# Kernel tuning notes

Measured on AMD Instinct MI355X. Metric: run time of the kernel, lower is better.

The kernel has to match this reference:

```python
import jax, jax.numpy as jnp
import numpy as np

B, N, C_S, C_COND, C_Z, H = 2, 512, 1024, 512, 128, 16
D = C_S // H  # head dim = 64
INF = 1.0e8
EPS = 1e-5


def _ln(x, scale=None, bias=None):
    m = x.mean(-1, keepdims=True)
    v = ((x - m) ** 2).mean(-1, keepdims=True)
    y = (x - m) * jax.lax.rsqrt(v + EPS)
    if scale is not None:
        y = y * scale + bias
    return y


def setup_inputs() -> dict:
    key = jax.random.key(0)
    ks = jax.random.split(key, 16)
    s = 0.02
    return {
        'x': jax.random.normal(ks[0], (B, N, C_S), jnp.float32),
        'cond': jax.random.normal(ks[1], (B, N, C_COND), jnp.float32),
        'z': jax.random.normal(ks[2], (B, N, N, C_Z), jnp.float32),
        'x_mask': jnp.ones((B, N), jnp.float32),
        # AdaLN(c_s, c_cond): scale/shift from cond
        'gamma_w': jax.random.normal(ks[3], (C_COND, C_S), jnp.float32) * s,
        'gamma_b': jnp.zeros((C_S,), jnp.float32),
        'beta_w': jax.random.normal(ks[4], (C_COND, C_S), jnp.float32) * s,
        # ln_z affine
        'z_scale': jnp.ones((C_Z,), jnp.float32),
        'z_bias': jnp.zeros((C_Z,), jnp.float32),
        # projections (all bias-free per module)
        'w_q': jax.random.normal(ks[5], (C_S, H * D), jnp.float32) * s,
        'w_kv': jax.random.normal(ks[6], (C_S, 2 * H * D), jnp.float32) * s,
        'w_b': jax.random.normal(ks[7], (C_Z, H), jnp.float32) * s,
        'w_og': jax.random.normal(ks[8], (C_S, C_S), jnp.float32) * s,
        'w_out': jax.random.normal(ks[9], (C_S, C_S), jnp.float32) * s,
        # cond_gate has bias, init -2.0
        'w_cg': jax.random.normal(ks[10], (C_COND, C_S), jnp.float32) * s,
        'b_cg': jnp.full((C_S,), -2.0, jnp.float32),
        # Transition (SwiGLU, n=2)
        'ffn_scale': jnp.ones((C_S,), jnp.float32),
        'ffn_bias': jnp.zeros((C_S,), jnp.float32),
        'w_a': jax.random.normal(ks[11], (C_S, 2 * C_S), jnp.float32) * s,
        'w_b2': jax.random.normal(ks[12], (C_S, 2 * C_S), jnp.float32) * s,
        'w_o': jax.random.normal(ks[13], (2 * C_S, C_S), jnp.float32) * s,
    }


def reference(x, cond, z, x_mask, gamma_w, gamma_b, beta_w, z_scale, z_bias,
              w_q, w_kv, w_b, w_og, w_out, w_cg, b_cg,
              ffn_scale, ffn_bias, w_a, w_b2, w_o):
    # AdaLN: LN(x, no affine) modulated by cond (sigmoid-gated scale + shift)
    cond_n = _ln(cond)
    _x = _ln(x) * jax.nn.sigmoid(cond_n @ gamma_w + gamma_b) + cond_n @ beta_w
    _z = _ln(z, z_scale, z_bias)

    q = (_x @ w_q).reshape(B, N, H, D)
    kv = _x @ w_kv
    k = kv[..., :H * D].reshape(B, N, H, D)
    v = kv[..., H * D:].reshape(B, N, H, D)

    # pair bias [B,N,N,H] -> [B,H,Nq,Nk], plus additive mask (query & key)
    b = _z @ w_b
    b = b + INF * (x_mask[:, None, :, None] - 1.0)  # key mask
    b = b + INF * (x_mask[:, :, None, None] - 1.0)  # query mask
    bias = jnp.transpose(b, (0, 3, 1, 2))  # [B,H,Nq,Nk]

    scale = 1.0 / jnp.sqrt(jnp.asarray(D, x.dtype))
    scores = jnp.einsum('bqhd,bkhd->bhqk', q, k) * scale + bias
    attn = jax.nn.softmax(scores, axis=-1)
    update = jnp.einsum('bhqk,bkhd->bqhd', attn, v).reshape(B, N, C_S)

    update = (update * jax.nn.sigmoid(_x @ w_og)) @ w_out
    update = update * jax.nn.sigmoid(cond @ w_cg + b_cg)
    x = x + update  # dropout is identity in eval

    # Transition (SwiGLU, n=2), masked residual
    xl = _ln(x, ffn_scale, ffn_bias)
    ffn = (jax.nn.silu(xl @ w_a) * (xl @ w_b2)) @ w_o
    x = x + ffn * x_mask[..., None]
    return x
```

## Files before the change

kernel.cpp:

```cpp
#include <hip/hip_runtime.h>
#include <stdint.h>

typedef unsigned short u16;
typedef unsigned int u32;
typedef __attribute__((ext_vector_type(4))) float f32x4;
typedef __attribute__((ext_vector_type(4))) unsigned int u32x4;
typedef __attribute__((ext_vector_type(4))) unsigned short u16x4;
typedef __attribute__((ext_vector_type(8))) __bf16 bf16x8;

union Frag { u32x4 u; bf16x8 b; };

__device__ __forceinline__ u16 f2bf(float x) {
  u32 u = __float_as_uint(x);
  u32 r = (u + 0x7fffu + ((u >> 16) & 1u)) >> 16;
  return (u16)r;
}
__device__ __forceinline__ float bf2f(u16 v) {
  u32 u = ((u32)v) << 16;
  return __uint_as_float(u);
}
__device__ __forceinline__ float sigmoidf_(float x) { return 1.0f / (1.0f + __expf(-x)); }

__device__ __forceinline__ void gload16(const void* g, void* lds) {
  __builtin_amdgcn_global_load_lds((const __attribute__((address_space(1))) unsigned int*)g,
                                   (__attribute__((address_space(3))) unsigned int*)lds, 16, 0, 0);
}

template<int EPI, int MI>
__device__ __forceinline__ void gemm_body(int bx, int by,
                                          u16* As0, u16* As1, u16* Bs0, u16* Bs1,
                                          const u16* __restrict__ A, const u16* __restrict__ Bt,
                                          const float* __restrict__ bias,
                                          const float* __restrict__ e0, const float* __restrict__ e1,
                                          void* __restrict__ Cp, int M, int N, int K) {
  constexpr int BM = 32 * MI;
  const int t = threadIdx.x, wave = t >> 6, lane = t & 63;
  const int lrow = lane & 15, lgrp = lane >> 4;
  const int m0 = bx * BM, n0 = by * 128;
  const int wr = (wave >> 1) * (16 * MI), wc = (wave & 1) * 64;

  const int srow = wave * 8 + (lane >> 3);
  const int scol = (((lane & 7) ^ (lane >> 3)) << 3);
  const u16* Ab = A + (size_t)(m0 + srow) * K + scol;
  const u16* Bb = Bt + (size_t)(n0 + srow) * K + scol;

  f32x4 acc[MI][4] = {};

  auto stage = [&](int k0, u16* Asd, u16* Bsd) {
#pragma unroll
    for (int i = 0; i < MI; ++i) gload16(Ab + (size_t)i * 32 * K + k0, Asd + wave * 512 + i * 2048);
#pragma unroll
    for (int i = 0; i < 4; ++i) gload16(Bb + (size_t)i * 32 * K + k0, Bsd + wave * 512 + i * 2048);
  };
  auto compute = [&](const u16* Asr, const u16* Bsr) {
#pragma unroll
    for (int ks = 0; ks < 2; ++ks) {
      Frag af[MI], bf4[4];
#pragma unroll
      for (int mi = 0; mi < MI; ++mi) {
        int row = wr + mi * 16 + lrow;
        int slot = ((ks << 2) + lgrp) ^ (row & 7);
        af[mi].u = *(const u32x4*)((const char*)Asr + row * 128 + (slot << 4));
      }
#pragma unroll
      for (int ni = 0; ni < 4; ++ni) {
        int row = wc + ni * 16 + lrow;
        int slot = ((ks << 2) + lgrp) ^ (row & 7);
        bf4[ni].u = *(const u32x4*)((const char*)Bsr + row * 128 + (slot << 4));
      }
#pragma unroll
      for (int mi = 0; mi < MI; ++mi)
#pragma unroll
        for (int ni = 0; ni < 4; ++ni)
          acc[mi][ni] = __builtin_amdgcn_mfma_f32_16x16x32_bf16(af[mi].b, bf4[ni].b, acc[mi][ni], 0, 0, 0);
    }
  };

  stage(0, As0, Bs0);
  __syncthreads();
  for (int k0 = 0; k0 < K; k0 += 128) {
    stage(k0 + 64, As1, Bs1);
    compute(As0, Bs0);
    __syncthreads();
    if (k0 + 128 < K) stage(k0 + 128, As0, Bs0);
    compute(As1, Bs1);
    __syncthreads();
  }

  if constexpr (EPI == 4 || EPI == 5) {
    const int half = N >> 1;
#pragma unroll
    for (int mi = 0; mi < MI; ++mi) {
#pragma unroll
      for (int np = 0; np < 2; ++np) {
        int j = ((n0 + wc) >> 1) + np * 16 + lrow;
        float bj = 0.0f;
        if (EPI == 5) bj = bias[j];
#pragma unroll
        for (int rg = 0; rg < 4; ++rg) {
          int row = m0 + wr + mi * 16 + lgrp * 4 + rg;
          float a = acc[mi][2 * np][rg];
          float b = acc[mi][2 * np + 1][rg];
          float val;
          if constexpr (EPI == 4) {
            val = a * sigmoidf_(a) * b;
          } else {
            float mean = e1[2 * row], rinv = e1[2 * row + 1];
            float lnx = (e0[(size_t)row * half + j] - mean) * rinv;
            val = lnx * sigmoidf_(a + bj) + b;
          }
          ((u16*)Cp)[(size_t)row * half + j] = f2bf(val);
        }
      }
    }
  } else if constexpr (EPI == 6) {
    u16* vTp = (u16*)bias;
    const bool isv = (n0 >= 2048) && (n0 < 3072);
#pragma unroll
    for (int mi = 0; mi < MI; ++mi) {
#pragma unroll
      for (int ni = 0; ni < 4; ++ni) {
        int col = n0 + wc + ni * 16 + lrow;
        int rowb = m0 + wr + mi * 16 + lgrp * 4;
        if (isv) {
          int h = (col - 2048) >> 6, d = col & 63;
          int b = rowb >> 9, n = rowb & 511;
          u16x4 o;
#pragma unroll
          for (int rg = 0; rg < 4; ++rg) o[rg] = f2bf(acc[mi][ni][rg]);
          *(u16x4*)(vTp + ((size_t)((b * 16 + h) * 64 + d)) * 512 + n) = o;
        } else {
#pragma unroll
          for (int rg = 0; rg < 4; ++rg)
            ((u16*)Cp)[(size_t)(rowb + rg) * N + col] = f2bf(acc[mi][ni][rg]);
        }
      }
    }
  } else {
#pragma unroll
    for (int mi = 0; mi < MI; ++mi) {
#pragma unroll
      for (int ni = 0; ni < 4; ++ni) {
        int col = n0 + wc + ni * 16 + lrow;
        float bv = 0.0f;
        if (EPI == 0 && bias) bv = bias[col];
#pragma unroll
        for (int rg = 0; rg < 4; ++rg) {
          int row = m0 + wr + mi * 16 + lgrp * 4 + rg;
          size_t idx = (size_t)row * N + col;
          float v = acc[mi][ni][rg];
          if constexpr (EPI == 0)      ((float*)Cp)[idx] = v + bv;
          else if constexpr (EPI == 1) ((u16*)Cp)[idx] = f2bf(v);
          else if constexpr (EPI == 2) ((float*)Cp)[idx] = e0[idx] + v * sigmoidf_(e1[idx]);
          else                         ((float*)Cp)[idx] = e0[idx] + v * e1[row];
        }
      }
    }
  }
  (void)M;
}

template<int EPI, int MI>
__global__ __launch_bounds__(256) void gemm_t(const u16* __restrict__ A, const u16* __restrict__ Bt,
                                              const float* __restrict__ bias,
                                              const float* __restrict__ e0, const float* __restrict__ e1,
                                              void* __restrict__ Cp, int M, int N, int K) {
  __shared__ u16 As0[32 * MI * 64], As1[32 * MI * 64];
  __shared__ u16 Bs0[128 * 64], Bs1[128 * 64];
  gemm_body<EPI, MI>(blockIdx.x, blockIdx.y, As0, As1, Bs0, Bs1, A, Bt, bias, e0, e1, Cp, M, N, K);
}

__global__ __launch_bounds__(256) void gemm_adaln_cg(
    const u16* __restrict__ cnb, const u16* __restrict__ gbT, const float* __restrict__ gamma_b,
    const float* __restrict__ x, const float* __restrict__ xstat, u16* __restrict__ xbf,
    const u16* __restrict__ cb, const u16* __restrict__ cgT, const float* __restrict__ b_cg,
    float* __restrict__ cglin) {
  __shared__ u16 As0[64 * 64], As1[64 * 64];
  __shared__ u16 Bs0[128 * 64], Bs1[128 * 64];
  int id = blockIdx.x;
  if (id < 256) {
    gemm_body<5, 2>(id & 15, id >> 4, As0, As1, Bs0, Bs1, cnb, gbT, gamma_b, x, xstat, xbf, 1024, 2048, 512);
  } else {
    id -= 256;
    gemm_body<0, 1>(id & 31, id >> 5, As0, As1, Bs0, Bs1, cb, cgT, b_cg, nullptr, nullptr, cglin, 1024, 1024, 512);
  }
}

__device__ __forceinline__ void wtrans_body(
    int id, float (*T)[65],
    const float* __restrict__ gamma_w, const float* __restrict__ beta_w,
    const float* __restrict__ w_cg, const float* __restrict__ w_q,
    const float* __restrict__ w_kv, const float* __restrict__ w_og,
    const float* __restrict__ w_out, const float* __restrict__ w_a,
    const float* __restrict__ w_b2, const float* __restrict__ w_o,
    u16* __restrict__ gbT, u16* __restrict__ cgT, u16* __restrict__ qkvT,
    u16* __restrict__ woT, u16* __restrict__ abT, u16* __restrict__ oT) {
  const float* src; u16* dst; int K, N, ptype = 0;
  if (id < 128)       { src = gamma_w; dst = gbT;  K = 512;  N = 1024; ptype = 1; }
  else if (id < 256)  { src = beta_w;  dst = gbT;  K = 512;  N = 1024; ptype = 2; id -= 128; }
  else if (id < 384)  { src = w_cg;    dst = cgT;  K = 512;  N = 1024; id -= 256; }
  else if (id < 640)  { src = w_q;     dst = qkvT; K = 1024; N = 1024; id -= 384; }
  else if (id < 1152) { src = w_kv;    dst = qkvT + (size_t)1024 * 1024; K = 1024; N = 2048; id -= 640; }
  else if (id < 1408) { src = w_og;    dst = qkvT + (size_t)3072 * 1024; K = 1024; N = 1024; id -= 1152; }
  else if (id < 1664) { src = w_out;   dst = woT;  K = 1024; N = 1024; id -= 1408; }
  else if (id < 2176) { src = w_a;     dst = abT;  K = 1024; N = 2048; ptype = 1; id -= 1664; }
  else if (id < 2688) { src = w_b2;    dst = abT;  K = 1024; N = 2048; ptype = 2; id -= 2176; }
  else                { src = w_o;     dst = oT;   K = 2048; N = 1024; id -= 2688; }
  const int tk = K >> 6;
  const int k0 = (id % tk) * 64, n0 = (id / tk) * 64;

  const int t = threadIdx.x;
#pragma unroll
  for (int i = 0; i < 4; ++i) {
    int idx = i * 256 + t;
    int kr = idx >> 4, c4 = (idx & 15) << 2;
    f32x4 v = *(const f32x4*)(src + (size_t)(k0 + kr) * N + n0 + c4);
    T[kr][c4] = v.x; T[kr][c4 + 1] = v.y; T[kr][c4 + 2] = v.z; T[kr][c4 + 3] = v.w;
  }
  __syncthreads();
#pragma unroll
  for (int i = 0; i < 2; ++i) {
    int idx = i * 256 + t;
    int n = idx >> 3, kc = (idx & 7) << 3;
    u32x4 o;
#pragma unroll
    for (int j = 0; j < 4; ++j) {
      u16 lo = f2bf(T[kc + 2 * j][n]);
      u16 hi = f2bf(T[kc + 2 * j + 1][n]);
      o[j] = (u32)lo | ((u32)hi << 16);
    }
    int ng = n0 + n;
    int r = (ptype == 0) ? ng : (((ng >> 4) << 5) + (ng & 15) + ((ptype == 2) ? 16 : 0));
    *(u32x4*)(dst + (size_t)r * K + k0 + kc) = o;
  }
}

__device__ __forceinline__ void block_reduce2_256(float& s, float& q, float* sb, int t) {
#pragma unroll
  for (int m = 1; m < 64; m <<= 1) { s += __shfl_xor(s, m); q += __shfl_xor(q, m); }
  if ((t & 63) == 0) { sb[(t >> 6) * 2] = s; sb[(t >> 6) * 2 + 1] = q; }
  __syncthreads();
  s = sb[0] + sb[2] + sb[4] + sb[6];
  q = sb[1] + sb[3] + sb[5] + sb[7];
}

__device__ __forceinline__ void ln_cond_x_body(int row, const float* __restrict__ cond,
                                               const float* __restrict__ x,
                                               u16* __restrict__ cnb, u16* __restrict__ cb,
                                               float* __restrict__ xstat) {
  const int t = threadIdx.x;
  __shared__ float sb[8];
  f32x4 xv = *(const f32x4*)(x + (size_t)row * 1024 + t * 4);
  float s = xv.x + xv.y + xv.z + xv.w;
  float q = xv.x * xv.x + xv.y * xv.y + xv.z * xv.z + xv.w * xv.w;
  block_reduce2_256(s, q, sb, t);
  if (t == 0) {
    float mean = s * (1.0f / 1024.0f);
    float var = q * (1.0f / 1024.0f) - mean * mean;
    xstat[2 * row] = mean;
    xstat[2 * row + 1] = rsqrtf(var + 1e-5f);
  }
  __syncthreads();
  f32x4 cv = {0.0f, 0.0f, 0.0f, 0.0f};
  if (t < 128) cv = *(const f32x4*)(cond + (size_t)row * 512 + t * 4);
  float s2 = cv.x + cv.y + cv.z + cv.w;
  float q2 = cv.x * cv.x + cv.y * cv.y + cv.z * cv.z + cv.w * cv.w;
  block_reduce2_256(s2, q2, sb, t);
  if (t < 128) {
    float mean = s2 * (1.0f / 512.0f);
    float var = q2 * (1.0f / 512.0f) - mean * mean;
    float rinv = rsqrtf(var + 1e-5f);
    u16x4 on, oc;
    on.x = f2bf((cv.x - mean) * rinv); on.y = f2bf((cv.y - mean) * rinv);
    on.z = f2bf((cv.z - mean) * rinv); on.w = f2bf((cv.w - mean) * rinv);
    oc.x = f2bf(cv.x); oc.y = f2bf(cv.y); oc.z = f2bf(cv.z); oc.w = f2bf(cv.w);
    *(u16x4*)(cnb + (size_t)row * 512 + t * 4) = on;
    *(u16x4*)(cb + (size_t)row * 512 + t * 4) = oc;
  }
}

__device__ __forceinline__ void biasz_body(int bq, const float* __restrict__ z,
                                           const float* __restrict__ zs, const float* __restrict__ zbias,
                                           const float* __restrict__ wb, const float* __restrict__ xmask,
                                           u16* __restrict__ biasb) {
  const int b = bq >> 9, qi = bq & 511;
  const int t = threadIdx.x, wave = t >> 6, lane = t & 63;
  const int lrow = lane & 15, lgrp = lane >> 4;

  float zsv[32], zbv[32];
  Frag wf[4];
#pragma unroll
  for (int j = 0; j < 4; ++j) {
#pragma unroll
    for (int e2 = 0; e2 < 4; ++e2) {
      int c0 = 32 * j + lgrp * 8 + e2 * 2;
      zsv[j * 8 + e2 * 2] = zs[c0];
      zsv[j * 8 + e2 * 2 + 1] = zs[c0 + 1];
      zbv[j * 8 + e2 * 2] = zbias[c0];
      zbv[j * 8 + e2 * 2 + 1] = zbias[c0 + 1];
      u16 lo = f2bf(wb[c0 * 16 + lrow]);
      u16 hi = f2bf(wb[(c0 + 1) * 16 + lrow]);
      wf[j].u[e2] = (u32)lo | ((u32)hi << 16);
    }
  }
  float qm = xmask[b * 512 + qi];
  float qadd = 1.0e8f * (qm - 1.0f);
  const float* zrowbase = z + ((size_t)(b * 512 + qi)) * 512 * 128;

  for (int kt = wave; kt < 32; kt += 4) {
    const float* zp = zrowbase + (size_t)(kt * 16 + lrow) * 128;
    float zv[32];
#pragma unroll
    for (int j = 0; j < 4; ++j) {
      f32x4 v0 = *(const f32x4*)(zp + 32 * j + lgrp * 8);
      f32x4 v1 = *(const f32x4*)(zp + 32 * j + lgrp * 8 + 4);
      zv[j * 8 + 0] = v0.x; zv[j * 8 + 1] = v0.y; zv[j * 8 + 2] = v0.z; zv[j * 8 + 3] = v0.w;
      zv[j * 8 + 4] = v1.x; zv[j * 8 + 5] = v1.y; zv[j * 8 + 6] = v1.z; zv[j * 8 + 7] = v1.w;
    }
    float s = 0.0f, q2 = 0.0f;
#pragma unroll
    for (int i = 0; i < 32; ++i) { s += zv[i]; q2 += zv[i] * zv[i]; }
    s += __shfl_xor(s, 16); q2 += __shfl_xor(q2, 16);
    s += __shfl_xor(s, 32); q2 += __shfl_xor(q2, 32);
    float mean = s * (1.0f / 128.0f);
    float var = q2 * (1.0f / 128.0f) - mean * mean;
    float rinv = rsqrtf(var + 1e-5f);

    f32x4 acc = {0.0f, 0.0f, 0.0f, 0.0f};
#pragma unroll
    for (int j = 0; j < 4; ++j) {
      Frag afr;
#pragma unroll
      for (int e2 = 0; e2 < 4; ++e2) {
        float zn0 = (zv[j * 8 + e2 * 2] - mean) * rinv * zsv[j * 8 + e2 * 2] + zbv[j * 8 + e2 * 2];
        float zn1 = (zv[j * 8 + e2 * 2 + 1] - mean) * rinv * zsv[j * 8 + e2 * 2 + 1] + zbv[j * 8 + e2 * 2 + 1];
        afr.u[e2] = (u32)f2bf(zn0) | ((u32)f2bf(zn1) << 16);
      }
      acc = __builtin_amdgcn_mfma_f32_16x16x32_bf16(afr.b, wf[j].b, acc, 0, 0, 0);
    }

    int kbase = kt * 16 + lgrp * 4;
    float v0 = acc[0] + qadd + 1.0e8f * (xmask[b * 512 + kbase + 0] - 1.0f);
    float v1 = acc[1] + qadd + 1.0e8f * (xmask[b * 512 + kbase + 1] - 1.0f);
    float v2 = acc[2] + qadd + 1.0e8f * (xmask[b * 512 + kbase + 2] - 1.0f);
    float v3 = acc[3] + qadd + 1.0e8f * (xmask[b * 512 + kbase + 3] - 1.0f);
    u16* outp = biasb + (((size_t)(b * 16 + lrow) * 512 + qi) * 512 + kbase);
    *(u32*)outp       = (u32)f2bf(v0) | ((u32)f2bf(v1) << 16);
    *(u32*)(outp + 2) = (u32)f2bf(v2) | ((u32)f2bf(v3) << 16);
  }
}

__global__ __launch_bounds__(256) void mega0(
    const float* __restrict__ z, const float* __restrict__ zs, const float* __restrict__ zbias,
    const float* __restrict__ wb, const float* __restrict__ xmask, u16* __restrict__ biasb,
    const float* __restrict__ gamma_w, const float* __restrict__ beta_w,
    const float* __restrict__ w_cg, const float* __restrict__ w_q,
    const float* __restrict__ w_kv, const float* __restrict__ w_og,
    const float* __restrict__ w_out, const float* __restrict__ w_a,
    const float* __restrict__ w_b2, const float* __restrict__ w_o,
    u16* __restrict__ gbT, u16* __restrict__ cgT, u16* __restrict__ qkvT,
    u16* __restrict__ woT, u16* __restrict__ abT, u16* __restrict__ oT,
    const float* __restrict__ cond, const float* __restrict__ x,
    u16* __restrict__ cnb, u16* __restrict__ cb, float* __restrict__ xstat) {
  __shared__ float Tsh[64][65];
  int id = blockIdx.x;
  if (id < 1024) {
    biasz_body(id, z, zs, zbias, wb, xmask, biasb);
  } else if (id < 4224) {
    wtrans_body(id - 1024, Tsh, gamma_w, beta_w, w_cg, w_q, w_kv, w_og, w_out, w_a, w_b2, w_o,
                gbT, cgT, qkvT, woT, abT, oT);
  } else {
    ln_cond_x_body(id - 4224, cond, x, cnb, cb, xstat);
  }
}

__global__ __launch_bounds__(256) void attn(const u16* __restrict__ qkv, const u16* __restrict__ vT,
                                            const u16* __restrict__ biasb, u16* __restrict__ gub) {
  __shared__ u16 Ks[64 * 64];
  __shared__ u16 Vs[64 * 64];
  __shared__ u16 Ps[4][16 * 64];
  __shared__ u16 Bbs[64 * 64];
  const int t = threadIdx.x, wave = t >> 6, lane = t & 63;
  const int lrow = lane & 15, lgrp = lane >> 4;
  const int bh = blockIdx.x >> 3, qt = blockIdx.x & 7;
  const int b = bh >> 4, h = bh & 15;
  const int q0 = qt * 64 + wave * 16;

  Frag qf[2];
#pragma unroll
  for (int ks = 0; ks < 2; ++ks) {
    int tok = b * 512 + q0 + lrow;
    qf[ks].u = *(const u32x4*)(qkv + (size_t)tok * 4096 + h * 64 + ks * 32 + lgrp * 8);
  }
  f32x4 oacc[4] = {};
  float mrun[4], lrun[4];
#pragma unroll
  for (int rg = 0; rg < 4; ++rg) { mrun[rg] = -3.0e38f; lrun[rg] = 0.0f; }

  const int o0 = t * 16, o1 = 4096 + t * 16;
  const int r0 = o0 >> 7, s0 = (o0 >> 4) & 7;
  const int r1 = o1 >> 7, s1 = (o1 >> 4) & 7;
  const int c0 = (s0 ^ (r0 & 7)) << 3;
  const int c1 = (s1 ^ (r1 & 7)) << 3;
  const int br0 = t >> 3, bs0 = t & 7;
  const int br1 = 32 + (t >> 3);
  const u16* bbase = biasb + ((size_t)bh * 512 + qt * 64) * 512;

  const u16* kp0 = qkv + (size_t)(b * 512 + r0) * 4096 + 1024 + h * 64 + c0;
  const u16* kp1 = qkv + (size_t)(b * 512 + r1) * 4096 + 1024 + h * 64 + c1;
  const u16* vp0 = vT + (size_t)(bh * 64 + r0) * 512 + c0;
  const u16* vp1 = vT + (size_t)(bh * 64 + r1) * 512 + c1;
  const u16* bp0 = bbase + (size_t)br0 * 512 + bs0 * 8;
  const u16* bp1 = bbase + (size_t)br1 * 512 + bs0 * 8;

  u32x4 kv0 = *(const u32x4*)(kp0);
  u32x4 kv1 = *(const u32x4*)(kp1);
  u32x4 vv0 = *(const u32x4*)(vp0);
  u32x4 vv1 = *(const u32x4*)(vp1);
  u32x4 bb0 = *(const u32x4*)(bp0);
  u32x4 bb1 = *(const u32x4*)(bp1);

  for (int kt = 0; kt < 8; ++kt) {
    __syncthreads();
    *(u32x4*)((char*)Ks + o0) = kv0;
    *(u32x4*)((char*)Ks + o1) = kv1;
    *(u32x4*)((char*)Vs + o0) = vv0;
    *(u32x4*)((char*)Vs + o1) = vv1;
    *(u32x4*)((char*)Bbs + br0 * 128 + ((bs0 ^ (br0 & 7)) << 4)) = bb0;
    *(u32x4*)((char*)Bbs + br1 * 128 + ((bs0 ^ (br1 & 7)) << 4)) = bb1;
    __syncthreads();

    {
      int k1g = ((kt + 1) & 7) * 64;
      kv0 = *(const u32x4*)(kp0 + (size_t)k1g * 4096);
      kv1 = *(const u32x4*)(kp1 + (size_t)k1g * 4096);
      vv0 = *(const u32x4*)(vp0 + k1g);
      vv1 = *(const u32x4*)(vp1 + k1g);
      bb0 = *(const u32x4*)(bp0 + k1g);
      bb1 = *(const u32x4*)(bp1 + k1g);
    }

    f32x4 sf[4] = {};
#pragma unroll
    for (int ks = 0; ks < 2; ++ks) {
#pragma unroll
      for (int ni = 0; ni < 4; ++ni) {
        int row = ni * 16 + lrow;
        int slot = (ks * 4 + lgrp) ^ (row & 7);
        Frag kf;
        kf.u = *(const u32x4*)((const char*)Ks + row * 128 + (slot << 4));
        sf[ni] = __builtin_amdgcn_mfma_f32_16x16x32_bf16(qf[ks].b, kf.b, sf[ni], 0, 0, 0);
      }
    }

    float sv[4][4];
#pragma unroll
    for (int ni = 0; ni < 4; ++ni) {
#pragma unroll
      for (int rg = 0; rg < 4; ++rg) {
        int qlocal = wave * 16 + lgrp * 4 + rg;
        int k = ni * 16 + lrow;
        float bvv = bf2f(*(const u16*)((const char*)Bbs + qlocal * 128 +
                                       (((k >> 3) ^ (qlocal & 7)) << 4) + (k & 7) * 2));
        sv[ni][rg] = sf[ni][rg] * 0.125f + bvv;
      }
    }
    float mnew[4], fac[4];
#pragma unroll
    for (int rg = 0; rg < 4; ++rg) {
      float tm = fmaxf(fmaxf(sv[0][rg], sv[1][rg]), fmaxf(sv[2][rg], sv[3][rg]));
      tm = fmaxf(tm, __shfl_xor(tm, 1));
      tm = fmaxf(tm, __shfl_xor(tm, 2));
      tm = fmaxf(tm, __shfl_xor(tm, 4));
      tm = fmaxf(tm, __shfl_xor(tm, 8));
      mnew[rg] = fmaxf(mrun[rg], tm);
      fac[rg] = __expf(mrun[rg] - mnew[rg]);
      mrun[rg] = mnew[rg];
    }
    float psum[4] = {0.0f, 0.0f, 0.0f, 0.0f};
#pragma unroll
    for (int ni = 0; ni < 4; ++ni)
#pragma unroll
      for (int rg = 0; rg < 4; ++rg) {
        float p = __expf(sv[ni][rg] - mnew[rg]);
        sv[ni][rg] = p;
        psum[rg] += p;
      }
#pragma unroll
    for (int rg = 0; rg < 4; ++rg) {
      float ps = psum[rg];
      ps += __shfl_xor(ps, 1); ps += __shfl_xor(ps, 2);
      ps += __shfl_xor(ps, 4); ps += __shfl_xor(ps, 8);
      lrun[rg] = lrun[rg] * fac[rg] + ps;
#pragma unroll
      for (int nd = 0; nd < 4; ++nd) oacc[nd][rg] *= fac[rg];
    }
#pragma unroll
    for (int ni = 0; ni < 4; ++ni)
#pragma unroll
      for (int rg = 0; rg < 4; ++rg) {
        int prow = lgrp * 4 + rg;
        int col = ni * 16 + lrow;
        int slot = (col >> 3) ^ (prow & 7);
        *(u16*)((char*)Ps[wave] + prow * 128 + (slot << 4) + (col & 7) * 2) = f2bf(sv[ni][rg]);
      }
    Frag paf[2];
#pragma unroll
    for (int ks = 0; ks < 2; ++ks) {
      int slot = (ks * 4 + lgrp) ^ (lrow & 7);
      paf[ks].u = *(const u32x4*)((const char*)Ps[wave] + lrow * 128 + (slot << 4));
    }
#pragma unroll
    for (int ks = 0; ks < 2; ++ks)
#pragma unroll
      for (int nd = 0; nd < 4; ++nd) {
        int row = nd * 16 + lrow;
        int slot = (ks * 4 + lgrp) ^ (row & 7);
        Frag vf;
        vf.u = *(const u32x4*)((const char*)Vs + row * 128 + (slot << 4));
        oacc[nd] = __builtin_amdgcn_mfma_f32_16x16x32_bf16(paf[ks].b, vf.b, oacc[nd], 0, 0, 0);
      }
  }

#pragma unroll
  for (int nd = 0; nd < 4; ++nd) {
#pragma unroll
    for (int rg = 0; rg < 4; ++rg) {
      int tok = b * 512 + q0 + lgrp * 4 + rg;
      int col = h * 64 + nd * 16 + lrow;
      float og = bf2f(qkv[(size_t)tok * 4096 + 3072 + col]);
      float val = oacc[nd][rg] / lrun[rg] * sigmoidf_(og);
      gub[(size_t)tok * 1024 + col] = f2bf(val);
    }
  }
}

__global__ __launch_bounds__(256) void ln_affine(const float* __restrict__ x1, const float* __restrict__ fs,
                                                 const float* __restrict__ fb, u16* __restrict__ xlb) {
  const int row = blockIdx.x;
  const int t = threadIdx.x;
  __shared__ float sb[8];
  f32x4 v = *(const f32x4*)(x1 + (size_t)row * 1024 + t * 4);
  float s = v.x + v.y + v.z + v.w;
  float q = v.x * v.x + v.y * v.y + v.z * v.z + v.w * v.w;
  block_reduce2_256(s, q, sb, t);
  float mean = s * (1.0f / 1024.0f);
  float var = q * (1.0f / 1024.0f) - mean * mean;
  float rinv = rsqrtf(var + 1e-5f);
  f32x4 fsv = *(const f32x4*)(fs + t * 4);
  f32x4 fbv = *(const f32x4*)(fb + t * 4);
  u16x4 o;
  o.x = f2bf((v.x - mean) * rinv * fsv.x + fbv.x);
  o.y = f2bf((v.y - mean) * rinv * fsv.y + fbv.y);
  o.z = f2bf((v.z - mean) * rinv * fsv.z + fbv.z);
  o.w = f2bf((v.w - mean) * rinv * fsv.w + fbv.w);
  *(u16x4*)(xlb + (size_t)row * 1024 + t * 4) = o;
}

extern "C" void kernel_launch(void* const* d_in, const int* in_sizes, int n_in,
                              void* d_out, int out_size, void* d_ws, size_t ws_size,
                              hipStream_t stream) {
  (void)in_sizes; (void)n_in; (void)out_size; (void)ws_size;
  const float* x        = (const float*)d_in[0];
  const float* cond     = (const float*)d_in[1];
  const float* z        = (const float*)d_in[2];
  const float* xmask    = (const float*)d_in[3];
  const float* gamma_w  = (const float*)d_in[4];
  const float* gamma_b  = (const float*)d_in[5];
  const float* beta_w   = (const float*)d_in[6];
  const float* z_scale  = (const float*)d_in[7];
  const float* z_bias   = (const float*)d_in[8];
  const float* w_q      = (const float*)d_in[9];
  const float* w_kv     = (const float*)d_in[10];
  const float* w_b      = (const float*)d_in[11];
  const float* w_og     = (const float*)d_in[12];
  const float* w_out    = (const float*)d_in[13];
  const float* w_cg     = (const float*)d_in[14];
  const float* b_cg     = (const float*)d_in[15];
  const float* ffn_scale= (const float*)d_in[16];
  const float* ffn_bias = (const float*)d_in[17];
  const float* w_a      = (const float*)d_in[18];
  const float* w_b2     = (const float*)d_in[19];
  const float* w_o      = (const float*)d_in[20];
  float* out = (float*)d_out;

  char* ws = (char*)d_ws;
  size_t off = 0;
  auto alloc = [&](size_t bytes) -> void* {
    void* p = ws + off;
    off += (bytes + 255) & ~(size_t)255;
    return p;
  };
  u16* cnb     = (u16*)alloc(1024 * 512 * 2);
  u16* cb      = (u16*)alloc(1024 * 512 * 2);
  float* xstat = (float*)alloc(1024 * 2 * 4);
  float* cglin = (float*)alloc((size_t)1024 * 1024 * 4);
  u16* xbf     = (u16*)alloc((size_t)1024 * 1024 * 2);
  u16* qkv     = (u16*)alloc((size_t)1024 * 4096 * 2);
  u16* vT      = (u16*)alloc((size_t)2048 * 512 * 2);
  u16* biasb   = (u16*)alloc((size_t)32 * 512 * 512 * 2);
  u16* gub     = (u16*)alloc((size_t)1024 * 1024 * 2);
  float* x1    = (float*)alloc((size_t)1024 * 1024 * 4);
  u16* xlb     = (u16*)alloc((size_t)1024 * 1024 * 2);
  u16* hb      = (u16*)alloc((size_t)1024 * 2048 * 2);
  u16* gbT     = (u16*)alloc((size_t)2048 * 512 * 2);
  u16* cgT     = (u16*)alloc((size_t)1024 * 512 * 2);
  u16* qkvT    = (u16*)alloc((size_t)4096 * 1024 * 2);
  u16* woT     = (u16*)alloc((size_t)1024 * 1024 * 2);
  u16* abT     = (u16*)alloc((size_t)4096 * 1024 * 2);
  u16* oT      = (u16*)alloc((size_t)1024 * 2048 * 2);

  mega0<<<5248, 256, 0, stream>>>(
      z, z_scale, z_bias, w_b, xmask, biasb,
      gamma_w, beta_w, w_cg, w_q, w_kv, w_og, w_out, w_a, w_b2, w_o,
      gbT, cgT, qkvT, woT, abT, oT,
      cond, x, cnb, cb, xstat);

  gemm_adaln_cg<<<512, 256, 0, stream>>>(cnb, gbT, gamma_b, x, xstat, xbf,
                                         cb, cgT, b_cg, cglin);

  gemm_t<6, 4><<<dim3(8, 32), 256, 0, stream>>>(xbf, qkvT, (const float*)vT, nullptr, nullptr,
                                                qkv, 1024, 4096, 1024);

  attn<<<256, 256, 0, stream>>>(qkv, vT, biasb, gub);

  gemm_t<2, 1><<<dim3(32, 8), 256, 0, stream>>>(gub, woT, nullptr, x, cglin, x1, 1024, 1024, 1024);

  ln_affine<<<1024, 256, 0, stream>>>(x1, ffn_scale, ffn_bias, xlb);

  gemm_t<4, 4><<<dim3(8, 32), 256, 0, stream>>>(xlb, abT, nullptr, nullptr, nullptr, hb, 1024, 4096, 1024);

  gemm_t<3, 1><<<dim3(32, 8), 256, 0, stream>>>(hb, oT, nullptr, x1, xmask, out, 1024, 1024, 2048);
}
```

Baseline: 176.1 us.

## Merge post-prep stages into one persistent kernel with global atomic barriers

Replaces the seven separate launches (AdaLN/cond-gate GEMM, QKV GEMM, attention, output GEMM, LayerNorm, two FFN GEMMs) with one persistent kernel of 256 blocks. The stages are separated by atomic-counter grid barriers, and the shared memory buffers are reused across stages. The goal is to remove kernel launch gaps and tail drain between stages. In exchange, stages that previously used 512 or 1024 blocks now run on only 256 blocks looping over the work. The plain (non-cooperative) launch relies on all 256 blocks being co-resident, and the 64KB of static shared memory per block limits occupancy to one block per CU.

New measurement: 343.3 us. 1.95x slower.

```diff
diff --git a/kernel.cpp b/kernel.cpp
--- a/kernel.cpp
+++ b/kernel.cpp
@@ -24,6 +24,20 @@
 __device__ __forceinline__ void gload16(const void* g, void* lds) {
   __builtin_amdgcn_global_load_lds((const __attribute__((address_space(1))) unsigned int*)g,
                                    (__attribute__((address_space(3))) unsigned int*)lds, 16, 0, 0);
+}
+
+#define NBLK 256
+__device__ __forceinline__ void gsync(unsigned* cnt) {
+  __syncthreads();
+  if (threadIdx.x == 0) {
+    __threadfence();
+    __hip_atomic_fetch_add(cnt, 1u, __ATOMIC_RELEASE, __HIP_MEMORY_SCOPE_AGENT);
+    while (__hip_atomic_load(cnt, __ATOMIC_ACQUIRE, __HIP_MEMORY_SCOPE_AGENT) < (unsigned)NBLK) {
+      __builtin_amdgcn_s_sleep(2);
+    }
+    __threadfence();
+  }
+  __syncthreads();
 }
 
 template<int EPI, int MI>
@@ -158,32 +172,6 @@
     }
   }
   (void)M;
-}
-
-template<int EPI, int MI>
-__global__ __launch_bounds__(256) void gemm_t(const u16* __restrict__ A, const u16* __restrict__ Bt,
-                                              const float* __restrict__ bias,
-                                              const float* __restrict__ e0, const float* __restrict__ e1,
-                                              void* __restrict__ Cp, int M, int N, int K) {
-  __shared__ u16 As0[32 * MI * 64], As1[32 * MI * 64];
-  __shared__ u16 Bs0[128 * 64], Bs1[128 * 64];
-  gemm_body<EPI, MI>(blockIdx.x, blockIdx.y, As0, As1, Bs0, Bs1, A, Bt, bias, e0, e1, Cp, M, N, K);
-}
-
-__global__ __launch_bounds__(256) void gemm_adaln_cg(
-    const u16* __restrict__ cnb, const u16* __restrict__ gbT, const float* __restrict__ gamma_b,
-    const float* __restrict__ x, const float* __restrict__ xstat, u16* __restrict__ xbf,
-    const u16* __restrict__ cb, const u16* __restrict__ cgT, const float* __restrict__ b_cg,
-    float* __restrict__ cglin) {
-  __shared__ u16 As0[64 * 64], As1[64 * 64];
-  __shared__ u16 Bs0[128 * 64], Bs1[128 * 64];
-  int id = blockIdx.x;
-  if (id < 256) {
-    gemm_body<5, 2>(id & 15, id >> 4, As0, As1, Bs0, Bs1, cnb, gbT, gamma_b, x, xstat, xbf, 1024, 2048, 512);
-  } else {
-    id -= 256;
-    gemm_body<0, 1>(id & 31, id >> 5, As0, As1, Bs0, Bs1, cb, cgT, b_cg, nullptr, nullptr, cglin, 1024, 1024, 512);
-  }
 }
 
 __device__ __forceinline__ void wtrans_body(
@@ -374,17 +362,15 @@
   }
 }
 
-__global__ __launch_bounds__(256) void attn(const u16* __restrict__ qkv, const u16* __restrict__ vT,
-                                            const u16* __restrict__ biasb, u16* __restrict__ gub) {
-  __shared__ u16 Ks[64 * 64];
-  __shared__ u16 Vs[64 * 64];
-  __shared__ u16 Ps[4][16 * 64];
-  __shared__ u16 Bbs[64 * 64];
+__device__ __forceinline__ void attn_body(int blk, u16* Ks, u16* Vs, u16* PsB, u16* Bbs,
+                                          const u16* __restrict__ qkv, const u16* __restrict__ vT,
+                                          const u16* __restrict__ biasb, u16* __restrict__ gub) {
   const int t = threadIdx.x, wave = t >> 6, lane = t & 63;
   const int lrow = lane & 15, lgrp = lane >> 4;
-  const int bh = blockIdx.x >> 3, qt = blockIdx.x & 7;
+  const int bh = blk >> 3, qt = blk & 7;
   const int b = bh >> 4, h = bh & 15;
   const int q0 = qt * 64 + wave * 16;
+  u16* PsW = PsB + wave * 1024;
 
   Frag qf[2];
 #pragma unroll
@@ -502,13 +488,13 @@
         int prow = lgrp * 4 + rg;
         int col = ni * 16 + lrow;
         int slot = (col >> 3) ^ (prow & 7);
-        *(u16*)((char*)Ps[wave] + prow * 128 + (slot << 4) + (col & 7) * 2) = f2bf(sv[ni][rg]);
+        *(u16*)((char*)PsW + prow * 128 + (slot << 4) + (col & 7) * 2) = f2bf(sv[ni][rg]);
       }
     Frag paf[2];
 #pragma unroll
     for (int ks = 0; ks < 2; ++ks) {
       int slot = (ks * 4 + lgrp) ^ (lrow & 7);
-      paf[ks].u = *(const u32x4*)((const char*)Ps[wave] + lrow * 128 + (slot << 4));
+      paf[ks].u = *(const u32x4*)((const char*)PsW + lrow * 128 + (slot << 4));
     }
 #pragma unroll
     for (int ks = 0; ks < 2; ++ks)
@@ -535,11 +521,10 @@
   }
 }
 
-__global__ __launch_bounds__(256) void ln_affine(const float* __restrict__ x1, const float* __restrict__ fs,
-                                                 const float* __restrict__ fb, u16* __restrict__ xlb) {
-  const int row = blockIdx.x;
+__device__ __forceinline__ void ln_affine_body(int row, const float* __restrict__ x1,
+                                               const float* __restrict__ fs, const float* __restrict__ fb,
+                                               u16* __restrict__ xlb, float* sb) {
   const int t = threadIdx.x;
-  __shared__ float sb[8];
   f32x4 v = *(const f32x4*)(x1 + (size_t)row * 1024 + t * 4);
   float s = v.x + v.y + v.z + v.w;
   float q = v.x * v.x + v.y * v.y + v.z * v.z + v.w * v.w;
@@ -555,6 +540,59 @@
   o.z = f2bf((v.z - mean) * rinv * fsv.z + fbv.z);
   o.w = f2bf((v.w - mean) * rinv * fsv.w + fbv.w);
   *(u16x4*)(xlb + (size_t)row * 1024 + t * 4) = o;
+}
+
+struct CoopArgs {
+  const u16* cnb; const u16* gbT; const float* gamma_b;
+  const float* x; const float* xstat; u16* xbf;
+  const u16* cb; const u16* cgT; const float* b_cg; float* cglin;
+  const u16* qkvT; u16* vT; u16* qkv;
+  const u16* biasb; u16* gub;
+  const u16* woT; float* x1;
+  const float* ffn_scale; const float* ffn_bias; u16* xlb;
+  const u16* abT; u16* hb;
+  const u16* oT; const float* xmask; float* out;
+  unsigned* bar;
+};
+
+__global__ __launch_bounds__(256, 1) void persist_main(CoopArgs a) {
+  __shared__ __attribute__((aligned(16))) char smem[65536];
+  u16* As0 = (u16*)smem;
+  u16* As1 = (u16*)(smem + 16384);
+  u16* Bs0 = (u16*)(smem + 32768);
+  u16* Bs1 = (u16*)(smem + 49152);
+  const int bid = blockIdx.x;
+
+  gemm_body<5, 2>(bid & 15, bid >> 4, As0, As1, Bs0, Bs1,
+                  a.cnb, a.gbT, a.gamma_b, a.x, a.xstat, a.xbf, 1024, 2048, 512);
+  gemm_body<0, 1>(bid & 31, bid >> 5, As0, As1, Bs0, Bs1,
+                  a.cb, a.cgT, a.b_cg, nullptr, nullptr, a.cglin, 1024, 1024, 512);
+  gsync(a.bar + 0);
+
+  gemm_body<6, 4>(bid & 7, bid >> 3, As0, As1, Bs0, Bs1,
+                  a.xbf, a.qkvT, (const float*)a.vT, nullptr, nullptr, a.qkv, 1024, 4096, 1024);
+  gsync(a.bar + 1);
+
+  attn_body(bid, (u16*)smem, (u16*)(smem + 8192), (u16*)(smem + 16384), (u16*)(smem + 24576),
+            a.qkv, a.vT, a.biasb, a.gub);
+  gsync(a.bar + 2);
+
+  gemm_body<2, 1>(bid & 31, bid >> 5, As0, As1, Bs0, Bs1,
+                  a.gub, a.woT, nullptr, a.x, a.cglin, a.x1, 1024, 1024, 1024);
+  gsync(a.bar + 3);
+
+  for (int r = bid; r < 1024; r += 256) {
+    ln_affine_body(r, a.x1, a.ffn_scale, a.ffn_bias, a.xlb, (float*)smem);
+    __syncthreads();
+  }
+  gsync(a.bar + 4);
+
+  gemm_body<4, 4>(bid & 7, bid >> 3, As0, As1, Bs0, Bs1,
+                  a.xlb, a.abT, nullptr, nullptr, nullptr, a.hb, 1024, 4096, 1024);
+  gsync(a.bar + 5);
+
+  gemm_body<3, 1>(bid & 31, bid >> 5, As0, As1, Bs0, Bs1,
+                  a.hb, a.oT, nullptr, a.x1, a.xmask, a.out, 1024, 1024, 2048);
 }
 
 extern "C" void kernel_launch(void* const* d_in, const int* in_sizes, int n_in,
@@ -609,6 +647,9 @@
   u16* woT     = (u16*)alloc((size_t)1024 * 1024 * 2);
   u16* abT     = (u16*)alloc((size_t)4096 * 1024 * 2);
   u16* oT      = (u16*)alloc((size_t)1024 * 2048 * 2);
+  unsigned* bar = (unsigned*)alloc(256);
+
+  hipMemsetAsync(bar, 0, 64, stream);
 
   mega0<<<5248, 256, 0, stream>>>(
       z, z_scale, z_bias, w_b, xmask, biasb,
@@ -616,19 +657,16 @@
       gbT, cgT, qkvT, woT, abT, oT,
       cond, x, cnb, cb, xstat);
 
-  gemm_adaln_cg<<<512, 256, 0, stream>>>(cnb, gbT, gamma_b, x, xstat, xbf,
-                                         cb, cgT, b_cg, cglin);
-
-  gemm_t<6, 4><<<dim3(8, 32), 256, 0, stream>>>(xbf, qkvT, (const float*)vT, nullptr, nullptr,
-                                                qkv, 1024, 4096, 1024);
-
-  attn<<<256, 256, 0, stream>>>(qkv, vT, biasb, gub);
-
-  gemm_t<2, 1><<<dim3(32, 8), 256, 0, stream>>>(gub, woT, nullptr, x, cglin, x1, 1024, 1024, 1024);
-
-  ln_affine<<<1024, 256, 0, stream>>>(x1, ffn_scale, ffn_bias, xlb);
-
-  gemm_t<4, 4><<<dim3(8, 32), 256, 0, stream>>>(xlb, abT, nullptr, nullptr, nullptr, hb, 1024, 4096, 1024);
-
-  gemm_t<3, 1><<<dim3(32, 8), 256, 0, stream>>>(hb, oT, nullptr, x1, xmask, out, 1024, 1024, 2048);
-}
+  CoopArgs ca;
+  ca.cnb = cnb; ca.gbT = gbT; ca.gamma_b = gamma_b;
+  ca.x = x; ca.xstat = xstat; ca.xbf = xbf;
+  ca.cb = cb; ca.cgT = cgT; ca.b_cg = b_cg; ca.cglin = cglin;
+  ca.qkvT = qkvT; ca.vT = vT; ca.qkv = qkv;
+  ca.biasb = biasb; ca.gub = gub;
+  ca.woT = woT; ca.x1 = x1;
+  ca.ffn_scale = ffn_scale; ca.ffn_bias = ffn_bias; ca.xlb = xlb;
+  ca.abT = abT; ca.hb = hb;
+  ca.oT = oT; ca.xmask = xmask; ca.out = out;
+  ca.bar = bar;
+  persist_main<<<NBLK, 256, 0, stream>>>(ca);
+}
```
